# Kernel tuning notes

Hardware: AMD Instinct MI355X
Metric: run time of the kernel (lower is better)

## Reference

```python
import jax, jax.numpy as jnp
import numpy as np

S, B, I, H, L = 512, 64, 128, 256, 6  # seq_len, batch, input, hidden, layers


def setup_inputs() -> dict:
    key = jax.random.key(0)
    ks = jax.random.split(key, 8)
    sc = 1.0 / np.sqrt(H)
    return {
        "x": jax.random.normal(ks[0], (S, B, I), jnp.float32),
        "h0": jax.random.normal(ks[1], (2 * L, B, H), jnp.float32),
        "w_ih0": jax.random.normal(ks[2], (2, 3 * H, I), jnp.float32) * sc,
        "b_ih0": jax.random.normal(ks[3], (2, 3 * H), jnp.float32) * sc,
        "w_ih": jax.random.normal(ks[4], (L - 1, 2, 3 * H, 2 * H), jnp.float32) * sc,
        "b_ih": jax.random.normal(ks[5], (L - 1, 2, 3 * H), jnp.float32) * sc,
        "w_hh": jax.random.normal(ks[6], (L, 2, 3 * H, H), jnp.float32) * sc,
        "b_hh": jax.random.normal(ks[7], (L, 2, 3 * H), jnp.float32) * sc,
    }


def _gru_direction(gi_seq, h0d, whh, bhh, reverse):
    # gi_seq: (S, B, 3H) precomputed input gates; h0d: (B, H)
    if reverse:
        gi_seq = gi_seq[::-1]

    def step(h, gi):
        gh = h @ whh.T + bhh                       # (B, 3H)
        gi_r, gi_z, gi_n = jnp.split(gi, 3, axis=-1)
        gh_r, gh_z, gh_n = jnp.split(gh, 3, axis=-1)
        r = jax.nn.sigmoid(gi_r + gh_r)
        z = jax.nn.sigmoid(gi_z + gh_z)
        n = jnp.tanh(gi_n + r * gh_n)
        h_new = (1.0 - z) * n + z * h
        return h_new, h_new

    h_n, outs = jax.lax.scan(step, h0d, gi_seq)
    if reverse:
        outs = outs[::-1]
    return h_n, outs  # (B,H), (S,B,H)


def reference(x, h0, w_ih0, b_ih0, w_ih, b_ih, w_hh, b_hh):
    cur = x
    finals = []
    for l in range(L):
        wi = w_ih0 if l == 0 else w_ih[l - 1]
        bi = b_ih0 if l == 0 else b_ih[l - 1]
        # precompute input-gate projections for the whole sequence (big GEMM)
        gi_f = jnp.einsum('sbi,gi->sbg', cur, wi[0]) + bi[0]
        gi_b = jnp.einsum('sbi,gi->sbg', cur, wi[1]) + bi[1]
        h_f, out_f = _gru_direction(gi_f, h0[2 * l], w_hh[l, 0], b_hh[l, 0], False)
        h_b, out_b = _gru_direction(gi_b, h0[2 * l + 1], w_hh[l, 1], b_hh[l, 1], True)
        finals.append(h_f)
        finals.append(h_b)
        if l < L - 1:
            cur = jnp.concatenate([out_f, out_b], axis=-1)  # (S, B, 2H)
    return jnp.stack(finals)  # (2L, B, H)
```

## Files before the change

kernel.cpp:

```cpp
#include <hip/hip_runtime.h>
#include <hip/hip_bf16.h>
#include <cstddef>

#define S_LEN 512
#define BATCH 64
#define HID 256
#define G3 768
#define SB (S_LEN*BATCH)
#define D2 512

typedef unsigned short u16;
typedef _Float16 h2v __attribute__((ext_vector_type(2)));
typedef __attribute__((ext_vector_type(8))) short s16x8;
typedef __attribute__((ext_vector_type(4))) float f32x4;

__device__ __forceinline__ float bf2f(u16 u) {
    return __uint_as_float(((unsigned)u) << 16);
}
__device__ __forceinline__ u16 f2bf(float f) {
    unsigned u = __float_as_uint(f);
    unsigned r = (u + 0x7FFFu + ((u >> 16) & 1u)) >> 16;
    return (u16)r;
}
__device__ __forceinline__ u16 f2h_bits(float f) {
    _Float16 h = (_Float16)f;
    union { _Float16 h; u16 u; } cv; cv.h = h;
    return cv.u;
}
__device__ __forceinline__ h2v u2h(unsigned u) {
    union { unsigned u; h2v h; } cv; cv.u = u;
    return cv.h;
}
__device__ __forceinline__ float dot2f(unsigned w, unsigned h, float acc) {
#if __has_builtin(__builtin_amdgcn_fdot2)
    return __builtin_amdgcn_fdot2(u2h(w), u2h(h), acc, false);
#else
    h2v wv = u2h(w), hv = u2h(h);
    return acc + (float)wv.x * (float)hv.x + (float)wv.y * (float)hv.y;
#endif
}
__device__ __forceinline__ float fast_rcp(float x) {
#if __has_builtin(__builtin_amdgcn_rcpf)
    return __builtin_amdgcn_rcpf(x);
#else
    return 1.f / x;
#endif
}
__device__ __forceinline__ void gload_lds16(const void* g, void* l) {
    __builtin_amdgcn_global_load_lds((const __attribute__((address_space(1))) void*)g,
                                     (__attribute__((address_space(3))) void*)l, 16, 0, 0);
}
__device__ __forceinline__ void bar_lgkm() {
    asm volatile("s_waitcnt lgkmcnt(0)" ::: "memory");
    __builtin_amdgcn_s_barrier();
    __builtin_amdgcn_sched_barrier(0);
}

__global__ void pack_whh_f16(const float* __restrict__ in, unsigned* __restrict__ out,
                             long total) {
    long i = (long)blockIdx.x * 256 + threadIdx.x;
    if (i >= total) return;
    long mat = i / (128L * G3);
    long rem = i - mat * (128L * G3);
    int k2 = (int)(rem / G3);
    int g  = (int)(rem - (long)k2 * G3);
    const float* base = in + mat * (768L * 256) + (long)g * 256 + 2 * k2;
    unsigned lo = f2h_bits(base[0]);
    unsigned hi = f2h_bits(base[1]);
    out[i] = lo | (hi << 16);
}

__global__ void f32_to_bf16(const float* __restrict__ in, u16* __restrict__ out, long n) {
    long i = (long)blockIdx.x * 256 + threadIdx.x;
    if (i < n) out[i] = f2bf(in[i]);
}

__global__ __launch_bounds__(256, 2) void gemm_mfma(
    const u16* __restrict__ A,
    const u16* __restrict__ Bt,
    const float* __restrict__ bias,
    u16* __restrict__ Cg,
    int K)
{
    int d = blockIdx.z;
    const u16* Bb = Bt + (size_t)d * 768 * K;
    const float* bi = bias + d * G3;
    u16* Cm = Cg + (size_t)d * SB * G3;

    int n0 = blockIdx.x * 128;
    int m0 = blockIdx.y * 128;
    int tid = threadIdx.x;
    int wave = tid >> 6, lane = tid & 63;
    int wm = wave >> 1, wn = wave & 1;

    __shared__ u16 Asm[128 * 32];
    __shared__ u16 Bsm[128 * 32];

    f32x4 acc[4][4] = {};

    for (int k0 = 0; k0 < K; k0 += 32) {
#pragma unroll
        for (int p = 0; p < 2; p++) {
            int c = p * 256 + wave * 64 + lane;
            int row = c >> 2, kc = c & 3;
            const u16* srcA = A + (size_t)(m0 + row) * K + k0 + kc * 8;
            const u16* srcB = Bb + (size_t)(n0 + row) * K + k0 + kc * 8;
            gload_lds16(srcA, &Asm[(p * 256 + wave * 64) * 8]);
            gload_lds16(srcB, &Bsm[(p * 256 + wave * 64) * 8]);
        }
        __syncthreads();

        s16x8 af[4], bfr[4];
#pragma unroll
        for (int i = 0; i < 4; i++) {
            int arow = wm * 64 + i * 16 + (lane & 15);
            af[i] = *reinterpret_cast<const s16x8*>(&Asm[arow * 32 + (lane >> 4) * 8]);
            int brow = wn * 64 + i * 16 + (lane & 15);
            bfr[i] = *reinterpret_cast<const s16x8*>(&Bsm[brow * 32 + (lane >> 4) * 8]);
        }
#pragma unroll
        for (int i = 0; i < 4; i++)
#pragma unroll
            for (int j = 0; j < 4; j++)
                acc[i][j] = __builtin_amdgcn_mfma_f32_16x16x32_bf16(af[i], bfr[j], acc[i][j], 0, 0, 0);
        __syncthreads();
    }

    int lcol = lane & 15, lrow4 = (lane >> 4) * 4;
#pragma unroll
    for (int i = 0; i < 4; i++) {
#pragma unroll
        for (int j = 0; j < 4; j++) {
            int n = n0 + wn * 64 + j * 16 + lcol;
            float bv = bi[n];
#pragma unroll
            for (int q = 0; q < 4; q++) {
                int m = m0 + wm * 64 + i * 16 + lrow4 + q;
                Cm[(size_t)m * G3 + n] = f2bf(acc[i][j][q] + bv);
            }
        }
    }
}

__global__ __launch_bounds__(768, 3) void gru_scan(
    const unsigned* __restrict__ wpack,
    const float* __restrict__ bhh,
    const u16* __restrict__ gi,
    const float* __restrict__ h0,
    u16* __restrict__ outc,
    float* __restrict__ finals,
    int layer)
{
    int b = blockIdx.x;
    int d = blockIdx.y;
    int tid = threadIdx.x;

    int ld = layer * 2 + d;
    const unsigned* Wp = wpack + (size_t)ld * 128 * G3 + tid;
    const u16* gid = gi + (size_t)d * SB * G3;

    __shared__ float gh_s[G3];
    __shared__ alignas(16) _Float16 h16_s[HID];
    __shared__ u16 gi_s[2][G3];

    unsigned wpk[128];
#pragma unroll
    for (int k = 0; k < 128; k++) wpk[k] = Wp[(size_t)k * G3];

    float bias_g = bhh[(size_t)ld * G3 + tid];

    float hreg = 0.f;
    if (tid < HID) {
        hreg = h0[(size_t)ld * BATCH * HID + b * HID + tid];
        h16_s[tid] = (_Float16)hreg;
    }
    {
        int s0 = d ? (S_LEN - 1) : 0;
        gi_s[0][tid] = gid[((size_t)s0 * BATCH + b) * G3 + tid];
    }
    __syncthreads();

    for (int t = 0; t < S_LEN; t++) {
        int s = d ? (S_LEN - 1 - t) : t;
        u16 ginext = 0;
        if (t + 1 < S_LEN) {
            int sn = d ? (s - 1) : (s + 1);
            ginext = gid[((size_t)sn * BATCH + b) * G3 + tid];
        }
        float accs[4];
        accs[0] = bias_g; accs[1] = 0.f; accs[2] = 0.f; accs[3] = 0.f;
        const uint4* hp = reinterpret_cast<const uint4*>(h16_s);
#pragma unroll
        for (int c = 0; c < 4; c++) {
            float a = accs[c];
#pragma unroll
            for (int u = 0; u < 8; u++) {
                uint4 q = hp[c * 8 + u];
                int base = 4 * (c * 8 + u);
                a = dot2f(wpk[base + 0], q.x, a);
                a = dot2f(wpk[base + 1], q.y, a);
                a = dot2f(wpk[base + 2], q.z, a);
                a = dot2f(wpk[base + 3], q.w, a);
            }
            accs[c] = a;
        }
        gh_s[tid] = (accs[0] + accs[1]) + (accs[2] + accs[3]);
        gi_s[(t + 1) & 1][tid] = ginext;
        bar_lgkm();
        if (tid < HID) {
            int j = tid;
            const u16* gs = gi_s[t & 1];
            float gir = bf2f(gs[j]);
            float giz = bf2f(gs[HID + j]);
            float gin = bf2f(gs[2 * HID + j]);
            float r = fast_rcp(1.f + __expf(-(gir + gh_s[j])));
            float z = fast_rcp(1.f + __expf(-(giz + gh_s[HID + j])));
            float xn = gin + r * gh_s[2 * HID + j];
            float e2 = __expf(2.f * xn);
            float n = 1.f - 2.f * fast_rcp(e2 + 1.f);
            float hn = (1.f - z) * n + z * hreg;
            hreg = hn;
            h16_s[j] = (_Float16)hn;
            if (outc) outc[((size_t)s * BATCH + b) * D2 + d * HID + j] = f2bf(hn);
        }
        bar_lgkm();
    }
    if (tid < HID)
        finals[(size_t)ld * BATCH * HID + b * HID + tid] = hreg;
}

extern "C" void kernel_launch(void* const* d_in, const int* in_sizes, int n_in,
                              void* d_out, int out_size, void* d_ws, size_t ws_size,
                              hipStream_t stream) {
    const float* x     = (const float*)d_in[0];
    const float* h0    = (const float*)d_in[1];
    const float* w_ih0 = (const float*)d_in[2];
    const float* b_ih0 = (const float*)d_in[3];
    const float* w_ih  = (const float*)d_in[4];
    const float* b_ih  = (const float*)d_in[5];
    const float* w_hh  = (const float*)d_in[6];
    const float* b_hh  = (const float*)d_in[7];
    float* out = (float*)d_out;

    char* ws = (char*)d_ws;
    unsigned* wpack = (unsigned*)(ws + 0);
    u16* wbf0 = (u16*)(ws + 4718592);
    u16* wbfl = (u16*)(ws + 5111808);
    u16* gi   = (u16*)(ws + 12976128);
    u16* curA = (u16*)(ws + 113639424);
    u16* curB = (u16*)(ws + 147193856);

    pack_whh_f16<<<(1179648 + 255) / 256, 256, 0, stream>>>(w_hh, wpack, 1179648L);
    f32_to_bf16<<<(196608 + 255) / 256, 256, 0, stream>>>(w_ih0, wbf0, 196608L);
    f32_to_bf16<<<(3932160 + 255) / 256, 256, 0, stream>>>(w_ih, wbfl, 3932160L);
    f32_to_bf16<<<(4194304 + 255) / 256, 256, 0, stream>>>(x, curA, 4194304L);

    u16* cin = curA;
    u16* cout_ = curB;
    for (int l = 0; l < 6; l++) {
        int K = l ? 512 : 128;
        const u16* wt = l ? (wbfl + (size_t)(l - 1) * 2 * 768 * 512) : wbf0;
        const float* bi = l ? (b_ih + (size_t)(l - 1) * 2 * 768) : b_ih0;
        dim3 g(6, 256, 2);
        gemm_mfma<<<g, 256, 0, stream>>>(cin, wt, bi, gi, K);
        gru_scan<<<dim3(64, 2), 768, 0, stream>>>(wpack, b_hh, gi, h0,
                                                  (l < 5) ? cout_ : (u16*)nullptr, out, l);
        u16* tmp = cin; cin = cout_; cout_ = tmp;
    }
}
```

Measured before the change: 4.163 ms.

## Rewrite GRU recurrence as batched MFMA scan with LDS-DMA gate prefetch

The per-sequence dot2 recurrence kernel (one block per batch element) is replaced by a scan in which each block handles 16 batch rows. The hidden-to-hidden product is computed with 16x16x32 f16 MFMA instructions, with the weight fragments held in registers. Input-gate tiles are prefetched into LDS through global_load_lds DMA, and the r/z recurrent biases are folded into the input GEMM bias, so only the n-gate bias stays in the scan. Only 8 blocks run instead of 128, and the large register-resident weight fragments risk spilling under the launch bounds.

```diff
diff --git a/kernel.cpp b/kernel.cpp
--- a/kernel.cpp
+++ b/kernel.cpp
@@ -10,8 +10,8 @@
 #define D2 512
 
 typedef unsigned short u16;
-typedef _Float16 h2v __attribute__((ext_vector_type(2)));
 typedef __attribute__((ext_vector_type(8))) short s16x8;
+typedef __attribute__((ext_vector_type(8))) _Float16 f16x8;
 typedef __attribute__((ext_vector_type(4))) float f32x4;
 
 __device__ __forceinline__ float bf2f(u16 u) {
@@ -21,23 +21,6 @@
     unsigned u = __float_as_uint(f);
     unsigned r = (u + 0x7FFFu + ((u >> 16) & 1u)) >> 16;
     return (u16)r;
-}
-__device__ __forceinline__ u16 f2h_bits(float f) {
-    _Float16 h = (_Float16)f;
-    union { _Float16 h; u16 u; } cv; cv.h = h;
-    return cv.u;
-}
-__device__ __forceinline__ h2v u2h(unsigned u) {
-    union { unsigned u; h2v h; } cv; cv.u = u;
-    return cv.h;
-}
-__device__ __forceinline__ float dot2f(unsigned w, unsigned h, float acc) {
-#if __has_builtin(__builtin_amdgcn_fdot2)
-    return __builtin_amdgcn_fdot2(u2h(w), u2h(h), acc, false);
-#else
-    h2v wv = u2h(w), hv = u2h(h);
-    return acc + (float)wv.x * (float)hv.x + (float)wv.y * (float)hv.y;
-#endif
 }
 __device__ __forceinline__ float fast_rcp(float x) {
 #if __has_builtin(__builtin_amdgcn_rcpf)
@@ -55,24 +38,26 @@
     __builtin_amdgcn_s_barrier();
     __builtin_amdgcn_sched_barrier(0);
 }
-
-__global__ void pack_whh_f16(const float* __restrict__ in, unsigned* __restrict__ out,
-                             long total) {
-    long i = (long)blockIdx.x * 256 + threadIdx.x;
-    if (i >= total) return;
-    long mat = i / (128L * G3);
-    long rem = i - mat * (128L * G3);
-    int k2 = (int)(rem / G3);
-    int g  = (int)(rem - (long)k2 * G3);
-    const float* base = in + mat * (768L * 256) + (long)g * 256 + 2 * k2;
-    unsigned lo = f2h_bits(base[0]);
-    unsigned hi = f2h_bits(base[1]);
-    out[i] = lo | (hi << 16);
+__device__ __forceinline__ void wait_vm0() {
+    asm volatile("s_waitcnt vmcnt(0)" ::: "memory");
 }
 
 __global__ void f32_to_bf16(const float* __restrict__ in, u16* __restrict__ out, long n) {
     long i = (long)blockIdx.x * 256 + threadIdx.x;
     if (i < n) out[i] = f2bf(in[i]);
+}
+__global__ void f32_to_f16(const float* __restrict__ in, _Float16* __restrict__ out, long n) {
+    long i = (long)blockIdx.x * 256 + threadIdx.x;
+    if (i < n) out[i] = (_Float16)in[i];
+}
+__global__ void add_bias(const float* __restrict__ bih0, const float* __restrict__ bihl,
+                         const float* __restrict__ bhh, float* __restrict__ outb) {
+    int i = blockIdx.x * 256 + threadIdx.x;
+    if (i >= 6 * 1536) return;
+    int l = i / 1536, r = i - l * 1536;
+    int g = r % 768;
+    float bi = (l == 0) ? bih0[r] : bihl[(l - 1) * 1536 + r];
+    outb[i] = bi + ((g < 512) ? bhh[i] : 0.f);
 }
 
 __global__ __launch_bounds__(256, 2) void gemm_mfma(
@@ -142,91 +127,126 @@
     }
 }
 
-__global__ __launch_bounds__(768, 3) void gru_scan(
-    const unsigned* __restrict__ wpack,
+__global__ __launch_bounds__(512, 2) void scan_mfma(
+    const _Float16* __restrict__ whh16,
+    const u16* __restrict__ gi,
     const float* __restrict__ bhh,
-    const u16* __restrict__ gi,
     const float* __restrict__ h0,
     u16* __restrict__ outc,
     float* __restrict__ finals,
     int layer)
 {
-    int b = blockIdx.x;
-    int d = blockIdx.y;
+    int b0 = blockIdx.x * 16;
+    int d  = blockIdx.y;
+    int ld = layer * 2 + d;
     int tid = threadIdx.x;
-
-    int ld = layer * 2 + d;
-    const unsigned* Wp = wpack + (size_t)ld * 128 * G3 + tid;
-    const u16* gid = gi + (size_t)d * SB * G3;
-
-    __shared__ float gh_s[G3];
-    __shared__ alignas(16) _Float16 h16_s[HID];
-    __shared__ u16 gi_s[2][G3];
-
-    unsigned wpk[128];
-#pragma unroll
-    for (int k = 0; k < 128; k++) wpk[k] = Wp[(size_t)k * G3];
-
-    float bias_g = bhh[(size_t)ld * G3 + tid];
-
-    float hreg = 0.f;
-    if (tid < HID) {
-        hreg = h0[(size_t)ld * BATCH * HID + b * HID + tid];
-        h16_s[tid] = (_Float16)hreg;
-    }
-    {
-        int s0 = d ? (S_LEN - 1) : 0;
-        gi_s[0][tid] = gid[((size_t)s0 * BATCH + b) * G3 + tid];
-    }
+    int wv = tid >> 6, lane = tid & 63;
+    int lr = lane & 15;
+    int lq = lane >> 4;
+    int r0 = lq * 4;
+
+    __shared__ alignas(16) _Float16 h_tiles[8][16][32];
+    __shared__ alignas(16) u16 gi_lds[2][16][G3];
+
+    const _Float16* Wl = whh16 + (size_t)ld * G3 * HID;
+    const u16* gid = gi + (size_t)d * (size_t)SB * G3;
+
+    f16x8 bfrag[6][8];
+#pragma unroll
+    for (int i = 0; i < 6; i++) {
+        int nt = (i & 1) ? (8 + wv) + (i >> 1) * 16 : wv + (i >> 1) * 16;
+        int g = nt * 16 + lr;
+#pragma unroll
+        for (int kt = 0; kt < 8; kt++)
+            bfrag[i][kt] = *reinterpret_cast<const f16x8*>(Wl + (size_t)g * HID + kt * 32 + lq * 8);
+    }
+
+    int c0 = wv * 16 + lr;
+    int c1 = (8 + wv) * 16 + lr;
+    float bhn0 = bhh[(size_t)ld * G3 + 2 * HID + c0];
+    float bhn1 = bhh[(size_t)ld * G3 + 2 * HID + c1];
+    float hreg0[4], hreg1[4];
+#pragma unroll
+    for (int q = 0; q < 4; q++) {
+        float hv0 = h0[(size_t)ld * BATCH * HID + (b0 + r0 + q) * HID + c0];
+        float hv1 = h0[(size_t)ld * BATCH * HID + (b0 + r0 + q) * HID + c1];
+        hreg0[q] = hv0; hreg1[q] = hv1;
+        h_tiles[c0 >> 5][r0 + q][c0 & 31] = (_Float16)hv0;
+        h_tiles[c1 >> 5][r0 + q][c1 & 31] = (_Float16)hv1;
+    }
+
+    auto dma_gi = [&](int s, int buf) {
+        const char* src = (const char*)(gid + ((size_t)s * BATCH + b0) * G3);
+        char* dst = (char*)&gi_lds[buf][0][0];
+#pragma unroll
+        for (int i = 0; i < 3; i++) {
+            int off = wv * 3072 + i * 1024;
+            gload_lds16(src + off + lane * 16, dst + off);
+        }
+    };
+
+    dma_gi(d ? (S_LEN - 1) : 0, 0);
+    wait_vm0();
     __syncthreads();
 
     for (int t = 0; t < S_LEN; t++) {
         int s = d ? (S_LEN - 1 - t) : t;
-        u16 ginext = 0;
-        if (t + 1 < S_LEN) {
-            int sn = d ? (s - 1) : (s + 1);
-            ginext = gid[((size_t)sn * BATCH + b) * G3 + tid];
-        }
-        float accs[4];
-        accs[0] = bias_g; accs[1] = 0.f; accs[2] = 0.f; accs[3] = 0.f;
-        const uint4* hp = reinterpret_cast<const uint4*>(h16_s);
-#pragma unroll
-        for (int c = 0; c < 4; c++) {
-            float a = accs[c];
-#pragma unroll
-            for (int u = 0; u < 8; u++) {
-                uint4 q = hp[c * 8 + u];
-                int base = 4 * (c * 8 + u);
-                a = dot2f(wpk[base + 0], q.x, a);
-                a = dot2f(wpk[base + 1], q.y, a);
-                a = dot2f(wpk[base + 2], q.z, a);
-                a = dot2f(wpk[base + 3], q.w, a);
+        int buf = t & 1;
+        if (t + 1 < S_LEN) dma_gi(d ? (s - 1) : (s + 1), buf ^ 1);
+
+        f32x4 acc[6] = {};
+#pragma unroll
+        for (int kt = 0; kt < 8; kt++) {
+            f16x8 a = *reinterpret_cast<const f16x8*>(&h_tiles[kt][lr][lq * 8]);
+#pragma unroll
+            for (int i = 0; i < 6; i++)
+                acc[i] = __builtin_amdgcn_mfma_f32_16x16x32_f16(a, bfrag[i][kt], acc[i], 0, 0, 0);
+        }
+        bar_lgkm();
+
+        const u16* gb = &gi_lds[buf][0][0];
+#pragma unroll
+        for (int q = 0; q < 4; q++) {
+            int row = r0 + q;
+            const u16* gr = gb + row * G3;
+            {
+                float gir = bf2f(gr[c0]);
+                float giz = bf2f(gr[HID + c0]);
+                float gin = bf2f(gr[2 * HID + c0]);
+                float r = fast_rcp(1.f + __expf(-(gir + acc[0][q])));
+                float z = fast_rcp(1.f + __expf(-(giz + acc[2][q])));
+                float xn = gin + r * (acc[4][q] + bhn0);
+                float e2 = __expf(2.f * xn);
+                float n = 1.f - 2.f * fast_rcp(e2 + 1.f);
+                float hn = (1.f - z) * n + z * hreg0[q];
+                hreg0[q] = hn;
+                h_tiles[c0 >> 5][row][c0 & 31] = (_Float16)hn;
+                if (outc) outc[((size_t)s * BATCH + b0 + row) * D2 + d * HID + c0] = f2bf(hn);
             }
-            accs[c] = a;
-        }
-        gh_s[tid] = (accs[0] + accs[1]) + (accs[2] + accs[3]);
-        gi_s[(t + 1) & 1][tid] = ginext;
+            {
+                float gir = bf2f(gr[c1]);
+                float giz = bf2f(gr[HID + c1]);
+                float gin = bf2f(gr[2 * HID + c1]);
+                float r = fast_rcp(1.f + __expf(-(gir + acc[1][q])));
+                float z = fast_rcp(1.f + __expf(-(giz + acc[3][q])));
+                float xn = gin + r * (acc[5][q] + bhn1);
+                float e2 = __expf(2.f * xn);
+                float n = 1.f - 2.f * fast_rcp(e2 + 1.f);
+                float hn = (1.f - z) * n + z * hreg1[q];
+                hreg1[q] = hn;
+                h_tiles[c1 >> 5][row][c1 & 31] = (_Float16)hn;
+                if (outc) outc[((size_t)s * BATCH + b0 + row) * D2 + d * HID + c1] = f2bf(hn);
+            }
+        }
+        wait_vm0();
         bar_lgkm();
-        if (tid < HID) {
-            int j = tid;
-            const u16* gs = gi_s[t & 1];
-            float gir = bf2f(gs[j]);
-            float giz = bf2f(gs[HID + j]);
-            float gin = bf2f(gs[2 * HID + j]);
-            float r = fast_rcp(1.f + __expf(-(gir + gh_s[j])));
-            float z = fast_rcp(1.f + __expf(-(giz + gh_s[HID + j])));
-            float xn = gin + r * gh_s[2 * HID + j];
-            float e2 = __expf(2.f * xn);
-            float n = 1.f - 2.f * fast_rcp(e2 + 1.f);
-            float hn = (1.f - z) * n + z * hreg;
-            hreg = hn;
-            h16_s[j] = (_Float16)hn;
-            if (outc) outc[((size_t)s * BATCH + b) * D2 + d * HID + j] = f2bf(hn);
-        }
-        bar_lgkm();
-    }
-    if (tid < HID)
-        finals[(size_t)ld * BATCH * HID + b * HID + tid] = hreg;
+    }
+
+#pragma unroll
+    for (int q = 0; q < 4; q++) {
+        finals[(size_t)ld * BATCH * HID + (b0 + r0 + q) * HID + c0] = hreg0[q];
+        finals[(size_t)ld * BATCH * HID + (b0 + r0 + q) * HID + c1] = hreg1[q];
+    }
 }
 
 extern "C" void kernel_launch(void* const* d_in, const int* in_sizes, int n_in,
@@ -243,27 +263,29 @@
     float* out = (float*)d_out;
 
     char* ws = (char*)d_ws;
-    unsigned* wpack = (unsigned*)(ws + 0);
-    u16* wbf0 = (u16*)(ws + 4718592);
-    u16* wbfl = (u16*)(ws + 5111808);
-    u16* gi   = (u16*)(ws + 12976128);
-    u16* curA = (u16*)(ws + 113639424);
-    u16* curB = (u16*)(ws + 147193856);
-
-    pack_whh_f16<<<(1179648 + 255) / 256, 256, 0, stream>>>(w_hh, wpack, 1179648L);
+    _Float16* whh16 = (_Float16*)(ws + 0);
+    u16* wbf0  = (u16*)(ws + 4718592);
+    u16* wbfl  = (u16*)(ws + 5111808);
+    float* biasT = (float*)(ws + 12976128);
+    u16* gi    = (u16*)(ws + 13012992);
+    u16* curA  = (u16*)(ws + 113676288);
+    u16* curB  = (u16*)(ws + 147230720);
+
+    f32_to_f16<<<(2359296 + 255) / 256, 256, 0, stream>>>(w_hh, whh16, 2359296L);
     f32_to_bf16<<<(196608 + 255) / 256, 256, 0, stream>>>(w_ih0, wbf0, 196608L);
     f32_to_bf16<<<(3932160 + 255) / 256, 256, 0, stream>>>(w_ih, wbfl, 3932160L);
     f32_to_bf16<<<(4194304 + 255) / 256, 256, 0, stream>>>(x, curA, 4194304L);
+    add_bias<<<(9216 + 255) / 256, 256, 0, stream>>>(b_ih0, b_ih, b_hh, biasT);
 
     u16* cin = curA;
     u16* cout_ = curB;
     for (int l = 0; l < 6; l++) {
         int K = l ? 512 : 128;
         const u16* wt = l ? (wbfl + (size_t)(l - 1) * 2 * 768 * 512) : wbf0;
-        const float* bi = l ? (b_ih + (size_t)(l - 1) * 2 * 768) : b_ih0;
+        const float* bi = biasT + (size_t)l * 1536;
         dim3 g(6, 256, 2);
         gemm_mfma<<<g, 256, 0, stream>>>(cin, wt, bi, gi, K);
-        gru_scan<<<dim3(64, 2), 768, 0, stream>>>(wpack, b_hh, gi, h0,
+        scan_mfma<<<dim3(4, 2), 512, 0, stream>>>(whh16, gi, b_hh, h0,
                                                   (l < 5) ? cout_ : (u16*)nullptr, out, l);
         u16* tmp = cin; cin = cout_; cout_ = tmp;
     }
```

Result: slower. 8.435 ms (+102.6%).
